# Kernel optimization log

Measured on AMD Instinct MI355X. Metric: run time of the kernel, lower is better.

The kernel has to match this reference:

```python
import jax, jax.numpy as jnp
import numpy as np

B, T, D = 2, 2048, 2048
H, KV = 16, 4
HD = D // H            # 128
N_REP = H // KV        # 4
KV_DIM = D * KV // H   # 512
ALIBI_W = 0.1


def _rotate_half(x):
    x1, x2 = jnp.split(x, 2, axis=-1)
    return jnp.concatenate([-x2, x1], axis=-1)


def _apply_rope(xq, xk, freqs_cis):
    # xq: [B,H,T,hd], xk: [B,KV,T,hd]; freqs_cis: [T, hd] (cos half | sin half)
    seq_len, head_dim = xq.shape[2], xq.shape[3]
    freqs = freqs_cis[:seq_len, :]
    half = head_dim // 2
    cos = jnp.repeat(freqs[:, :half], 2, axis=-1)[None, None]  # [1,1,T,hd]
    sin = jnp.repeat(freqs[:, half:], 2, axis=-1)[None, None]
    xq_out = xq * cos + _rotate_half(xq) * sin
    xk_out = xk * cos + _rotate_half(xk) * sin
    return xq_out, xk_out


def setup_inputs() -> dict:
    key = jax.random.key(0)
    ks = jax.random.split(key, 8)
    x = jax.random.normal(ks[0], (B, T, D), jnp.float32)
    # additive causal mask (0 on/below diag, -1e9 above)
    causal = jnp.tril(jnp.ones((T, T), jnp.bool_))
    mask = jnp.where(causal, 0.0, -1e9).astype(jnp.float32)[None, None]
    # RoPE table: first half cos, second half sin of t*theta
    inv_freq = 1.0 / (10000.0 ** (np.arange(0, HD, 2, dtype=np.float32) / HD))  # [hd/2]
    angles = jnp.arange(T, dtype=jnp.float32)[:, None] * jnp.asarray(inv_freq)[None, :]
    freqs_cis = jnp.concatenate([jnp.cos(angles), jnp.sin(angles)], axis=-1)  # [T, hd]
    # ALiBi bias: per-head slope * relative distance
    slopes = 2.0 ** (-8.0 * (jnp.arange(1, H + 1, dtype=jnp.float32) / H))  # [H]
    rel = (jnp.arange(T, dtype=jnp.float32)[None, :] - jnp.arange(T, dtype=jnp.float32)[:, None])
    alibi_bias = (-jnp.abs(rel)[None, None] * slopes[None, :, None, None]).astype(jnp.float32)
    std = 0.02
    Wq = std * jax.random.normal(ks[1], (D, D), jnp.float32)
    Wk = std * jax.random.normal(ks[2], (D, KV_DIM), jnp.float32)
    Wv = std * jax.random.normal(ks[3], (D, KV_DIM), jnp.float32)
    Wo = std * jax.random.normal(ks[4], (D, D), jnp.float32)
    return {"x": x, "mask": mask, "freqs_cis": freqs_cis, "alibi_bias": alibi_bias,
            "Wq": Wq, "Wk": Wk, "Wv": Wv, "Wo": Wo}


def reference(x, mask, freqs_cis, alibi_bias, Wq, Wk, Wv, Wo):
    b, t, d = x.shape
    q = (x @ Wq).reshape(b, t, H, HD).transpose(0, 2, 1, 3)      # [B,H,T,hd]
    k = (x @ Wk).reshape(b, t, KV, HD).transpose(0, 2, 1, 3)     # [B,KV,T,hd]
    v = (x @ Wv).reshape(b, t, KV, HD).transpose(0, 2, 1, 3)     # [B,KV,T,hd]
    q, k = _apply_rope(q, k, freqs_cis)
    # grouped-query scores: group query heads by kv head, avoid repeating K/V
    qg = q.reshape(b, KV, N_REP, t, HD)
    scores = jnp.einsum('bgrtd,bgsd->bgrts', qg, k) / jnp.sqrt(jnp.float32(HD))
    alibi = alibi_bias[:, :, :t, :t].reshape(1, KV, N_REP, t, t)
    scores = scores * (1.0 - ALIBI_W) + alibi * ALIBI_W
    scores = scores + mask[:, :, None, :t, :t]                   # broadcast [1,1,1,T,T]
    attn = jax.nn.softmax(scores.astype(jnp.float32), axis=-1).astype(x.dtype)
    out = jnp.einsum('bgrts,bgsd->bgrtd', attn, v)               # [B,KV,n_rep,T,hd]
    out = out.reshape(b, H, t, HD).transpose(0, 2, 1, 3).reshape(b, t, d)
    return out @ Wo
```

## Files before the change

kernel.cpp:

```cpp
#include <hip/hip_runtime.h>

#define T_SEQ 2048
#define D_MODEL 2048
#define NH 16
#define NKV 4
#define HEAD_DIM 128

typedef unsigned short u16;
typedef __attribute__((ext_vector_type(8))) short bf16x8;
typedef __attribute__((ext_vector_type(4))) float f32x4;

__device__ __forceinline__ float bf2f(u16 u) { return __uint_as_float(((unsigned)u) << 16); }
__device__ __forceinline__ u16 f2bf(float f) {
  unsigned x = __float_as_uint(f);
  return (u16)((x + 0x7FFFu + ((x >> 16) & 1u)) >> 16);
}
__device__ __forceinline__ float fexp2(float x) { return __builtin_amdgcn_exp2f(x); }

#define ASYNC_COPY16(g, l)                                                        \
  __builtin_amdgcn_global_load_lds((const __attribute__((address_space(1))) unsigned int*)(g), \
                                   (__attribute__((address_space(3))) unsigned int*)(l), 16, 0, 0)

#define BARRIER() do { asm volatile("" ::: "memory"); __builtin_amdgcn_s_barrier(); asm volatile("" ::: "memory"); } while (0)

template<int N> __device__ __forceinline__ void vmwait() {
  if constexpr (N == 0) asm volatile("s_waitcnt vmcnt(0)" ::: "memory");
  else if constexpr (N == 3) asm volatile("s_waitcnt vmcnt(3)" ::: "memory");
  else if constexpr (N == 4) asm volatile("s_waitcnt vmcnt(4)" ::: "memory");
  else if constexpr (N == 5) asm volatile("s_waitcnt vmcnt(5)" ::: "memory");
}

__global__ void cast_kernel(const float* __restrict__ x, u16* __restrict__ y, int n4) {
  int i = blockIdx.x * 256 + threadIdx.x;
  if (i >= n4) return;
  const float4 v = reinterpret_cast<const float4*>(x)[i];
  unsigned p0 = (unsigned)f2bf(v.x) | ((unsigned)f2bf(v.y) << 16);
  unsigned p1 = (unsigned)f2bf(v.z) | ((unsigned)f2bf(v.w) << 16);
  reinterpret_cast<uint2*>(y)[i] = make_uint2(p0, p1);
}

__global__ void transpose4_kernel(const float* __restrict__ Wq, const float* __restrict__ Wk,
                                  const float* __restrict__ Wv, const float* __restrict__ Wo,
                                  u16* __restrict__ qkvT, u16* __restrict__ WoT) {
  __shared__ float t[32][33];
  const int m = blockIdx.z;
  const float* W; u16* WT; int N;
  if (m == 0)      { W = Wq; WT = qkvT;                         N = 2048; }
  else if (m == 1) { W = Wk; WT = qkvT + (size_t)2048 * 2048;   N = 512;  }
  else if (m == 2) { W = Wv; WT = qkvT + (size_t)2560 * 2048;   N = 512;  }
  else             { W = Wo; WT = WoT;                          N = 2048; }
  const int n0 = blockIdx.x * 32, k0 = blockIdx.y * 32;
  if (n0 >= N) return;
  const int tx = threadIdx.x, ty = threadIdx.y;
#pragma unroll
  for (int i = 0; i < 32; i += 8)
    t[ty + i][tx] = W[(size_t)(k0 + ty + i) * N + n0 + tx];
  __syncthreads();
#pragma unroll
  for (int i = 0; i < 32; i += 8)
    WT[(size_t)(n0 + ty + i) * 2048 + k0 + tx] = f2bf(t[tx][ty + i]);
}

__global__ void vt_kernel(const u16* __restrict__ vb, u16* __restrict__ vt, int vstride) {
  __shared__ u16 t[32][33];
  const int bg = blockIdx.z;
  const int b = bg >> 2, g = bg & 3;
  const int t0 = blockIdx.x * 32, n0 = blockIdx.y * 32;
  const int tx = threadIdx.x, ty = threadIdx.y;
#pragma unroll
  for (int i = 0; i < 32; i += 8)
    t[ty + i][tx] = vb[((size_t)(b * T_SEQ + t0 + ty + i)) * vstride + g * HEAD_DIM + n0 + tx];
  __syncthreads();
#pragma unroll
  for (int i = 0; i < 32; i += 8)
    vt[((size_t)(bg * HEAD_DIM + n0 + ty + i)) * T_SEQ + t0 + tx] = t[tx][ty + i];
}

template<int BM, int BN, int WM, int WN, int EA, int EB, int OUT_BF16>
__global__ __launch_bounds__(512, 1) void gemm_dp(const u16* __restrict__ A, const u16* __restrict__ BT,
                                                  void* __restrict__ Cv, int M, int N, int K, int nbx) {
  constexpr int PA = BM / 64, PB = BN / 64;
  constexpr int E = EA + EB;
  constexpr int FM = BM / WM / 16, FN = BN / WN / 16;
  static_assert(FM % 2 == 0 && FN % 2 == 0, "quadrant split");
  __shared__ u16 SA[2][BM * 64];
  __shared__ u16 SB[2][BN * 64];
  const int tid = threadIdx.x;
  const int wave = tid >> 6, lane = tid & 63;
  const int lr = lane & 15, lg = lane >> 4;
  const int wm = wave / WN, wn = wave % WN;
  const int nwg = gridDim.x;
  const int bid = blockIdx.x;
  const int swz = (bid & 7) * (nwg >> 3) + (bid >> 3);
  const int bx = swz % nbx, by = swz / nbx;
  const size_t arow0 = (size_t)by * BM;
  const size_t brow0 = (size_t)bx * BN;
  const int NT = K >> 6;

  const int srow = tid >> 3;
  const int scol = ((tid & 7) ^ (srow & 7)) << 3;

  f32x4 acc[FM][FN] = {};
  bf16x8 af[FM / 2][2], bf0[FN / 2][2], bf1[FN / 2][2];

  const u16* Abase = A + arow0 * K;
  const u16* Bbase = BT + brow0 * K;

  auto stageA = [&](int p, int ktile, int buf) {
    if (ktile >= NT) return;
    const u16* src = Abase + (size_t)(p * 64 + srow) * K + (ktile << 6) + scol;
    ASYNC_COPY16(src, &SA[buf][(p * 64 + wave * 8) * 64]);
  };
  auto stageB = [&](int p, int ktile, int buf) {
    if (ktile >= NT) return;
    const u16* src = Bbase + (size_t)(p * 64 + srow) * K + (ktile << 6) + scol;
    ASYNC_COPY16(src, &SB[buf][(p * 64 + wave * 8) * 64]);
  };
  auto ldA = [&](int c, int mh) {
#pragma unroll
    for (int mf = 0; mf < FM / 2; ++mf)
#pragma unroll
      for (int ks = 0; ks < 2; ++ks) {
        const int row = wm * (BM / WM) + (mh * (FM / 2) + mf) * 16 + lr;
        const int slot = ((ks << 2) | lg) ^ (lr & 7);
        af[mf][ks] = *reinterpret_cast<const bf16x8*>(&SA[c][row * 64 + (slot << 3)]);
      }
  };
  auto ldB = [&](int c, int nh, bf16x8 (*bfr)[2]) {
#pragma unroll
    for (int nf = 0; nf < FN / 2; ++nf)
#pragma unroll
      for (int ks = 0; ks < 2; ++ks) {
        const int row = wn * (BN / WN) + (nh * (FN / 2) + nf) * 16 + lr;
        const int slot = ((ks << 2) | lg) ^ (lr & 7);
        bfr[nf][ks] = *reinterpret_cast<const bf16x8*>(&SB[c][row * 64 + (slot << 3)]);
      }
  };
  auto mq = [&](int mh, int nh, bf16x8 (*bfr)[2]) {
    __builtin_amdgcn_s_setprio(1);
#pragma unroll
    for (int mf = 0; mf < FM / 2; ++mf)
#pragma unroll
      for (int nf = 0; nf < FN / 2; ++nf)
#pragma unroll
        for (int ks = 0; ks < 2; ++ks)
          acc[mh * (FM / 2) + mf][nh * (FN / 2) + nf] = __builtin_amdgcn_mfma_f32_16x16x32_bf16(
              af[mf][ks], bfr[nf][ks], acc[mh * (FM / 2) + mf][nh * (FN / 2) + nf], 0, 0, 0);
    __builtin_amdgcn_s_setprio(0);
  };

#pragma unroll
  for (int p = 0; p < PA; ++p) stageA(p, 0, 0);
#pragma unroll
  for (int p = 0; p < PB; ++p) stageB(p, 0, 0);
#pragma unroll
  for (int p = 0; p < EB; ++p) stageB(p, 1, 1);
#pragma unroll
  for (int p = 0; p < EA; ++p) stageA(p, 1, 1);
  vmwait<E>();
  BARRIER();

  for (int kt = 0; kt < NT; ++kt) {
    const int c = kt & 1;
    ldA(c, 0); ldB(c, 0, bf0);
#pragma unroll
    for (int p = EB; p < PB; ++p) stageB(p, kt + 1, c ^ 1);
    BARRIER();
    mq(0, 0, bf0);
    BARRIER();
    ldB(c, 1, bf1);
#pragma unroll
    for (int p = EA; p < PA; ++p) stageA(p, kt + 1, c ^ 1);
    BARRIER();
    mq(0, 1, bf1);
    BARRIER();
    ldA(c, 1);
#pragma unroll
    for (int p = 0; p < EB; ++p) stageB(p, kt + 2, c);
    BARRIER();
    mq(1, 1, bf1);
    BARRIER();
#pragma unroll
    for (int p = 0; p < EA; ++p) stageA(p, kt + 2, c);
    BARRIER();
    mq(1, 0, bf0);
    if (kt + 2 < NT) vmwait<E>(); else vmwait<0>();
    BARRIER();
  }

#pragma unroll
  for (int mf = 0; mf < FM; ++mf)
#pragma unroll
    for (int nf = 0; nf < FN; ++nf)
#pragma unroll
      for (int r = 0; r < 4; ++r) {
        size_t row = arow0 + wm * (BM / WM) + mf * 16 + lg * 4 + r;
        size_t col = brow0 + wn * (BN / WN) + nf * 16 + lr;
        if (OUT_BF16) ((u16*)Cv)[row * N + col] = f2bf(acc[mf][nf][r]);
        else          ((float*)Cv)[row * N + col] = acc[mf][nf][r];
      }
}

__global__ void rope2_kernel(u16* __restrict__ qkv, const float* __restrict__ freqs) {
  const int QT = 4096 * NH * 64;
  int idx = blockIdx.x * 256 + threadIdx.x;
  u16* p; int log2nh;
  if (idx < QT) { p = qkv; log2nh = 4; }
  else          { p = qkv + 2048; log2nh = 2; idx -= QT; }
  int d = idx & 63;
  int h = (idx >> 6) & ((1 << log2nh) - 1);
  int row = idx >> (6 + log2nh);
  int t = row & (T_SEQ - 1);
  size_t base = (size_t)row * 3072 + (size_t)h * 128;
  float x1 = bf2f(p[base + d]);
  float x2 = bf2f(p[base + 64 + d]);
  const float* fr = freqs + (size_t)t * 128;
  int dh = d >> 1;
  float c1 = fr[dh],      s1 = fr[64 + dh];
  float c2 = fr[32 + dh], s2 = fr[96 + dh];
  p[base + d]      = f2bf(x1 * c1 - x2 * s1);
  p[base + 64 + d] = f2bf(x2 * c2 + x1 * s2);
}

__global__ __launch_bounds__(512) void attn_kernel(const u16* __restrict__ q, const u16* __restrict__ k,
                                                   const u16* __restrict__ vt, u16* __restrict__ o,
                                                   int qstride, int kstride) {
  __shared__ u16 Kl[2][64][136];
  __shared__ u16 Vl[2][128][72];
  __shared__ u16 Pl[8][16][72];
  const int b = blockIdx.z, h = blockIdx.y, pairIdx = blockIdx.x;
  const int g = h >> 2;
  const int tid = threadIdx.x, wave = tid >> 6, lane = tid & 63;
  const int lr = lane & 15, lg = lane >> 4;

  const float LOG2E = 1.44269504089f;
  const float qk_scale = 0.9f / sqrtf(128.f) * LOG2E;
  const float slope2   = 0.1f * fexp2(-0.5f * (h + 1)) * LOG2E;
  const float THR = 16.0f;

  const int krow = tid >> 3, kc0 = (tid & 7) * 16;
  const int vrow = tid >> 2, vc0 = (tid & 3) * 16;
  const u16* kbp = k + ((size_t)(b * T_SEQ + krow)) * kstride + g * HEAD_DIM + kc0;
  const u16* vbp = vt + ((size_t)((b * NKV + g) * HEAD_DIM + vrow)) * T_SEQ + vc0;

  float cb[4];
#pragma unroll
  for (int nt = 0; nt < 4; ++nt) cb[nt] = slope2 * (float)(nt * 16 + lr);

  for (int half = 0; half < 2; ++half) {
    const int qt = half ? (15 - pairIdx) : pairIdx;
    const int qbase = qt * 128;

    const u16* qp = q + ((size_t)(b * T_SEQ + qbase + wave * 16 + lr)) * qstride + h * HEAD_DIM;
    bf16x8 qf[4];
#pragma unroll
    for (int ks = 0; ks < 4; ++ks) qf[ks] = *reinterpret_cast<const bf16x8*>(qp + ks * 32 + lg * 8);

    f32x4 oa[8] = {};
    float m_r[4], l_r[4];
#pragma unroll
    for (int r = 0; r < 4; ++r) { m_r[r] = -1e30f; l_r[r] = 0.f; }

    const int ktmax = 2 * qt + 1;
    const int irow_min_w = qbase + wave * 16;
    const int irow_max_w = irow_min_w + 15;
    int cur = 0;

    __syncthreads();
    {
      bf16x8 k0a = *reinterpret_cast<const bf16x8*>(kbp);
      bf16x8 k0b = *reinterpret_cast<const bf16x8*>(kbp + 8);
      bf16x8 v0a = *reinterpret_cast<const bf16x8*>(vbp);
      bf16x8 v0b = *reinterpret_cast<const bf16x8*>(vbp + 8);
      *reinterpret_cast<bf16x8*>(&Kl[0][krow][kc0]) = k0a;
      *reinterpret_cast<bf16x8*>(&Kl[0][krow][kc0 + 8]) = k0b;
      *reinterpret_cast<bf16x8*>(&Vl[0][vrow][vc0]) = v0a;
      *reinterpret_cast<bf16x8*>(&Vl[0][vrow][vc0 + 8]) = v0b;
    }

    for (int kt = 0; kt <= ktmax; ++kt) {
      const int kbase = kt * 64;
      __syncthreads();

      const bool pf = (kt < ktmax);
      bf16x8 pk0, pk1, pv0, pv1;
      if (pf) {
        const u16* ks2p = kbp + (size_t)(kbase + 64) * kstride;
        pk0 = *reinterpret_cast<const bf16x8*>(ks2p);
        pk1 = *reinterpret_cast<const bf16x8*>(ks2p + 8);
        const u16* vs2p = vbp + kbase + 64;
        pv0 = *reinterpret_cast<const bf16x8*>(vs2p);
        pv1 = *reinterpret_cast<const bf16x8*>(vs2p + 8);
      }

      const bool compute = (kbase <= irow_max_w);
      if (compute) {
        f32x4 sa[4] = {};
#pragma unroll
        for (int nt = 0; nt < 4; ++nt)
#pragma unroll
          for (int ks = 0; ks < 4; ++ks)
            sa[nt] = __builtin_amdgcn_mfma_f32_16x16x32_bf16(
                qf[ks], *reinterpret_cast<const bf16x8*>(&Kl[cur][nt * 16 + lr][ks * 32 + lg * 8]), sa[nt], 0, 0, 0);

        const int i_row0 = irow_min_w + lg * 4;
        const float tb = slope2 * (float)kbase;
        float sv[4][4];
        float pmx[4] = {-1e30f, -1e30f, -1e30f, -1e30f};
        if (kbase + 63 <= irow_min_w) {
#pragma unroll
          for (int nt = 0; nt < 4; ++nt) {
            const float bias = cb[nt] + tb;
#pragma unroll
            for (int r = 0; r < 4; ++r) {
              float xv = fmaf(sa[nt][r], qk_scale, bias);
              sv[nt][r] = xv;
              pmx[r] = fmaxf(pmx[r], xv);
            }
          }
        } else {
#pragma unroll
          for (int nt = 0; nt < 4; ++nt) {
            const int jcol = kbase + nt * 16 + lr;
            const float bias = cb[nt] + tb;
#pragma unroll
            for (int r = 0; r < 4; ++r) {
              float xv = (jcol <= i_row0 + r) ? fmaf(sa[nt][r], qk_scale, bias) : -1e30f;
              sv[nt][r] = xv;
              pmx[r] = fmaxf(pmx[r], xv);
            }
          }
        }

        bool okl = true;
#pragma unroll
        for (int r = 0; r < 4; ++r) okl = okl && (pmx[r] <= m_r[r] + THR);
        if (__all(okl)) {
          float rs[4] = {0.f, 0.f, 0.f, 0.f};
#pragma unroll
          for (int nt = 0; nt < 4; ++nt)
#pragma unroll
            for (int r = 0; r < 4; ++r) {
              float p = fexp2(sv[nt][r] - m_r[r]);
              sv[nt][r] = p;
              rs[r] += p;
            }
#pragma unroll
          for (int r = 0; r < 4; ++r) l_r[r] += rs[r];
        } else {
#pragma unroll
          for (int mm = 1; mm < 16; mm <<= 1)
#pragma unroll
            for (int r = 0; r < 4; ++r) pmx[r] = fmaxf(pmx[r], __shfl_xor(pmx[r], mm, 64));
          float corr[4], rs[4];
#pragma unroll
          for (int r = 0; r < 4; ++r) {
            float mn = fmaxf(m_r[r], pmx[r]);
            corr[r] = fexp2(m_r[r] - mn);
            m_r[r] = mn;
            rs[r] = 0.f;
          }
#pragma unroll
          for (int nt = 0; nt < 4; ++nt)
#pragma unroll
            for (int r = 0; r < 4; ++r) {
              float p = fexp2(sv[nt][r] - m_r[r]);
              sv[nt][r] = p;
              rs[r] += p;
            }
#pragma unroll
          for (int r = 0; r < 4; ++r) l_r[r] = l_r[r] * corr[r] + rs[r];
#pragma unroll
          for (int t8 = 0; t8 < 8; ++t8)
#pragma unroll
            for (int r = 0; r < 4; ++r) oa[t8][r] *= corr[r];
        }

#pragma unroll
        for (int nt = 0; nt < 4; ++nt)
#pragma unroll
          for (int r = 0; r < 4; ++r)
            Pl[wave][lg * 4 + r][nt * 16 + lr] = f2bf(sv[nt][r]);
      }

      if (pf) {
        *reinterpret_cast<bf16x8*>(&Kl[cur ^ 1][krow][kc0]) = pk0;
        *reinterpret_cast<bf16x8*>(&Kl[cur ^ 1][krow][kc0 + 8]) = pk1;
        *reinterpret_cast<bf16x8*>(&Vl[cur ^ 1][vrow][vc0]) = pv0;
        *reinterpret_cast<bf16x8*>(&Vl[cur ^ 1][vrow][vc0 + 8]) = pv1;
      }

      if (compute) {
#pragma unroll
        for (int ht = 0; ht < 8; ++ht)
#pragma unroll
          for (int ks2 = 0; ks2 < 2; ++ks2) {
            bf16x8 pa = *reinterpret_cast<const bf16x8*>(&Pl[wave][lr][ks2 * 32 + lg * 8]);
            bf16x8 vb8 = *reinterpret_cast<const bf16x8*>(&Vl[cur][ht * 16 + lr][ks2 * 32 + lg * 8]);
            oa[ht] = __builtin_amdgcn_mfma_f32_16x16x32_bf16(pa, vb8, oa[ht], 0, 0, 0);
          }
      }
      cur ^= 1;
    }

#pragma unroll
    for (int mm = 1; mm < 16; mm <<= 1)
#pragma unroll
      for (int r = 0; r < 4; ++r) l_r[r] += __shfl_xor(l_r[r], mm, 64);

    u16* op = o + ((size_t)(b * T_SEQ + qbase + wave * 16)) * D_MODEL + h * HEAD_DIM;
#pragma unroll
    for (int r = 0; r < 4; ++r) {
      float inv = 1.0f / l_r[r];
#pragma unroll
      for (int ht = 0; ht < 8; ++ht)
        op[(size_t)(lg * 4 + r) * D_MODEL + ht * 16 + lr] = f2bf(oa[ht][r] * inv);
    }
  }
}

extern "C" void kernel_launch(void* const* d_in, const int* in_sizes, int n_in,
                              void* d_out, int out_size, void* d_ws, size_t ws_size,
                              hipStream_t stream) {
  (void)in_sizes; (void)n_in; (void)out_size; (void)ws_size;
  const float* x     = (const float*)d_in[0];
  const float* freqs = (const float*)d_in[2];
  const float* Wq    = (const float*)d_in[4];
  const float* Wk    = (const float*)d_in[5];
  const float* Wv    = (const float*)d_in[6];
  const float* Wo    = (const float*)d_in[7];
  float* out = (float*)d_out;
  char* ws = (char*)d_ws;
  const size_t MB = 1024 * 1024;
  u16* xb   = (u16*)(ws);
  u16* qkvT = (u16*)(ws + 16 * MB);
  u16* WoT  = (u16*)(ws + 28 * MB);
  u16* qkv  = (u16*)(ws + 36 * MB);
  u16* vtb  = (u16*)(ws + 16 * MB);
  const int M = 2 * T_SEQ;
  const int NQKV = 3072;

  cast_kernel<<<(M * D_MODEL / 4 + 255) / 256, 256, 0, stream>>>(x, xb, M * D_MODEL / 4);
  dim3 tb(32, 8);
  transpose4_kernel<<<dim3(64, 64, 4), tb, 0, stream>>>(Wq, Wk, Wv, Wo, qkvT, WoT);

  gemm_dp<256, 192, 4, 2, 2, 2, 1><<<256, 512, 0, stream>>>(xb, qkvT, qkv, M, NQKV, 2048, NQKV / 192);

  rope2_kernel<<<(M * NH * 64 + M * NKV * 64) / 256, 256, 0, stream>>>(qkv, freqs);

  vt_kernel<<<dim3(T_SEQ / 32, HEAD_DIM / 32, 2 * NKV), tb, 0, stream>>>(qkv + 2560, vtb, NQKV);

  attn_kernel<<<dim3(8, NH, 2), 512, 0, stream>>>(qkv, qkv + 2048, vtb, xb, NQKV, NQKV);

  gemm_dp<128, 256, 2, 4, 1, 2, 0><<<256, 512, 0, stream>>>(xb, WoT, out, M, 2048, 2048, 2048 / 256);
}
```

Before: 212.0 us.

## Process both paired query tiles in one K/V sweep to share loads

The attention kernel previously handled the two paired query tiles (pairIdx and 15-pairIdx) one after another, streaming K/V through LDS twice. Now both tiles' accumulators live in registers at once, and a single K/V loop up to the larger tile's causal limit serves both. The aim is to roughly halve K/V global loads, LDS fills and barriers for the shorter tile. The cost is doubled accumulator and Q register state (two sets of oa, m, l, qf), which raises register pressure and may reduce occupancy or cause spills.

```diff
diff --git a/kernel.cpp b/kernel.cpp
--- a/kernel.cpp
+++ b/kernel.cpp
@@ -247,175 +247,288 @@
 #pragma unroll
   for (int nt = 0; nt < 4; ++nt) cb[nt] = slope2 * (float)(nt * 16 + lr);
 
-  for (int half = 0; half < 2; ++half) {
-    const int qt = half ? (15 - pairIdx) : pairIdx;
-    const int qbase = qt * 128;
-
-    const u16* qp = q + ((size_t)(b * T_SEQ + qbase + wave * 16 + lr)) * qstride + h * HEAD_DIM;
-    bf16x8 qf[4];
-#pragma unroll
-    for (int ks = 0; ks < 4; ++ks) qf[ks] = *reinterpret_cast<const bf16x8*>(qp + ks * 32 + lg * 8);
-
-    f32x4 oa[8] = {};
-    float m_r[4], l_r[4];
-#pragma unroll
-    for (int r = 0; r < 4; ++r) { m_r[r] = -1e30f; l_r[r] = 0.f; }
-
-    const int ktmax = 2 * qt + 1;
-    const int irow_min_w = qbase + wave * 16;
-    const int irow_max_w = irow_min_w + 15;
-    int cur = 0;
-
+  const int qtA = pairIdx, qtB = 15 - pairIdx;
+  const int qbaseA = qtA * 128, qbaseB = qtB * 128;
+
+  const u16* qpA = q + ((size_t)(b * T_SEQ + qbaseA + wave * 16 + lr)) * qstride + h * HEAD_DIM;
+  const u16* qpB = q + ((size_t)(b * T_SEQ + qbaseB + wave * 16 + lr)) * qstride + h * HEAD_DIM;
+  bf16x8 qfA[4], qfB[4];
+#pragma unroll
+  for (int ks = 0; ks < 4; ++ks) {
+    qfA[ks] = *reinterpret_cast<const bf16x8*>(qpA + ks * 32 + lg * 8);
+    qfB[ks] = *reinterpret_cast<const bf16x8*>(qpB + ks * 32 + lg * 8);
+  }
+
+  f32x4 oaA[8] = {}, oaB[8] = {};
+  float mA[4], lA[4], mB[4], lB[4];
+#pragma unroll
+  for (int r = 0; r < 4; ++r) { mA[r] = -1e30f; lA[r] = 0.f; mB[r] = -1e30f; lB[r] = 0.f; }
+
+  const int ktmaxB = 2 * qtB + 1;
+  const int irowminA = qbaseA + wave * 16, irowmaxA = irowminA + 15;
+  const int irowminB = qbaseB + wave * 16, irowmaxB = irowminB + 15;
+  int cur = 0;
+
+  {
+    bf16x8 k0a = *reinterpret_cast<const bf16x8*>(kbp);
+    bf16x8 k0b = *reinterpret_cast<const bf16x8*>(kbp + 8);
+    bf16x8 v0a = *reinterpret_cast<const bf16x8*>(vbp);
+    bf16x8 v0b = *reinterpret_cast<const bf16x8*>(vbp + 8);
+    *reinterpret_cast<bf16x8*>(&Kl[0][krow][kc0]) = k0a;
+    *reinterpret_cast<bf16x8*>(&Kl[0][krow][kc0 + 8]) = k0b;
+    *reinterpret_cast<bf16x8*>(&Vl[0][vrow][vc0]) = v0a;
+    *reinterpret_cast<bf16x8*>(&Vl[0][vrow][vc0 + 8]) = v0b;
+  }
+
+  for (int kt = 0; kt <= ktmaxB; ++kt) {
+    const int kbase = kt * 64;
     __syncthreads();
-    {
-      bf16x8 k0a = *reinterpret_cast<const bf16x8*>(kbp);
-      bf16x8 k0b = *reinterpret_cast<const bf16x8*>(kbp + 8);
-      bf16x8 v0a = *reinterpret_cast<const bf16x8*>(vbp);
-      bf16x8 v0b = *reinterpret_cast<const bf16x8*>(vbp + 8);
-      *reinterpret_cast<bf16x8*>(&Kl[0][krow][kc0]) = k0a;
-      *reinterpret_cast<bf16x8*>(&Kl[0][krow][kc0 + 8]) = k0b;
-      *reinterpret_cast<bf16x8*>(&Vl[0][vrow][vc0]) = v0a;
-      *reinterpret_cast<bf16x8*>(&Vl[0][vrow][vc0 + 8]) = v0b;
+
+    const bool pf = (kt < ktmaxB);
+    bf16x8 pk0, pk1, pv0, pv1;
+    if (pf) {
+      const u16* ks2p = kbp + (size_t)(kbase + 64) * kstride;
+      pk0 = *reinterpret_cast<const bf16x8*>(ks2p);
+      pk1 = *reinterpret_cast<const bf16x8*>(ks2p + 8);
+      const u16* vs2p = vbp + kbase + 64;
+      pv0 = *reinterpret_cast<const bf16x8*>(vs2p);
+      pv1 = *reinterpret_cast<const bf16x8*>(vs2p + 8);
     }
 
-    for (int kt = 0; kt <= ktmax; ++kt) {
-      const int kbase = kt * 64;
-      __syncthreads();
-
-      const bool pf = (kt < ktmax);
-      bf16x8 pk0, pk1, pv0, pv1;
-      if (pf) {
-        const u16* ks2p = kbp + (size_t)(kbase + 64) * kstride;
-        pk0 = *reinterpret_cast<const bf16x8*>(ks2p);
-        pk1 = *reinterpret_cast<const bf16x8*>(ks2p + 8);
-        const u16* vs2p = vbp + kbase + 64;
-        pv0 = *reinterpret_cast<const bf16x8*>(vs2p);
-        pv1 = *reinterpret_cast<const bf16x8*>(vs2p + 8);
-      }
-
-      const bool compute = (kbase <= irow_max_w);
-      if (compute) {
-        f32x4 sa[4] = {};
+    const float tb = slope2 * (float)kbase;
+
+    const bool cA = (kbase <= irowmaxA);
+    if (cA) {
+      f32x4 sa[4] = {};
+#pragma unroll
+      for (int nt = 0; nt < 4; ++nt)
+#pragma unroll
+        for (int ks = 0; ks < 4; ++ks)
+          sa[nt] = __builtin_amdgcn_mfma_f32_16x16x32_bf16(
+              qfA[ks], *reinterpret_cast<const bf16x8*>(&Kl[cur][nt * 16 + lr][ks * 32 + lg * 8]), sa[nt], 0, 0, 0);
+
+      const int i_row0 = irowminA + lg * 4;
+      float sv[4][4];
+      float pmx[4] = {-1e30f, -1e30f, -1e30f, -1e30f};
+      if (kbase + 63 <= irowminA) {
+#pragma unroll
+        for (int nt = 0; nt < 4; ++nt) {
+          const float bias = cb[nt] + tb;
+#pragma unroll
+          for (int r = 0; r < 4; ++r) {
+            float xv = fmaf(sa[nt][r], qk_scale, bias);
+            sv[nt][r] = xv;
+            pmx[r] = fmaxf(pmx[r], xv);
+          }
+        }
+      } else {
+#pragma unroll
+        for (int nt = 0; nt < 4; ++nt) {
+          const int jcol = kbase + nt * 16 + lr;
+          const float bias = cb[nt] + tb;
+#pragma unroll
+          for (int r = 0; r < 4; ++r) {
+            float xv = (jcol <= i_row0 + r) ? fmaf(sa[nt][r], qk_scale, bias) : -1e30f;
+            sv[nt][r] = xv;
+            pmx[r] = fmaxf(pmx[r], xv);
+          }
+        }
+      }
+
+      bool okl = true;
+#pragma unroll
+      for (int r = 0; r < 4; ++r) okl = okl && (pmx[r] <= mA[r] + THR);
+      if (__all(okl)) {
+        float rs[4] = {0.f, 0.f, 0.f, 0.f};
 #pragma unroll
         for (int nt = 0; nt < 4; ++nt)
 #pragma unroll
-          for (int ks = 0; ks < 4; ++ks)
-            sa[nt] = __builtin_amdgcn_mfma_f32_16x16x32_bf16(
-                qf[ks], *reinterpret_cast<const bf16x8*>(&Kl[cur][nt * 16 + lr][ks * 32 + lg * 8]), sa[nt], 0, 0, 0);
-
-        const int i_row0 = irow_min_w + lg * 4;
-        const float tb = slope2 * (float)kbase;
-        float sv[4][4];
-        float pmx[4] = {-1e30f, -1e30f, -1e30f, -1e30f};
-        if (kbase + 63 <= irow_min_w) {
-#pragma unroll
-          for (int nt = 0; nt < 4; ++nt) {
-            const float bias = cb[nt] + tb;
-#pragma unroll
-            for (int r = 0; r < 4; ++r) {
-              float xv = fmaf(sa[nt][r], qk_scale, bias);
-              sv[nt][r] = xv;
-              pmx[r] = fmaxf(pmx[r], xv);
-            }
-          }
-        } else {
-#pragma unroll
-          for (int nt = 0; nt < 4; ++nt) {
-            const int jcol = kbase + nt * 16 + lr;
-            const float bias = cb[nt] + tb;
-#pragma unroll
-            for (int r = 0; r < 4; ++r) {
-              float xv = (jcol <= i_row0 + r) ? fmaf(sa[nt][r], qk_scale, bias) : -1e30f;
-              sv[nt][r] = xv;
-              pmx[r] = fmaxf(pmx[r], xv);
-            }
-          }
-        }
-
-        bool okl = true;
-#pragma unroll
-        for (int r = 0; r < 4; ++r) okl = okl && (pmx[r] <= m_r[r] + THR);
-        if (__all(okl)) {
-          float rs[4] = {0.f, 0.f, 0.f, 0.f};
-#pragma unroll
-          for (int nt = 0; nt < 4; ++nt)
-#pragma unroll
-            for (int r = 0; r < 4; ++r) {
-              float p = fexp2(sv[nt][r] - m_r[r]);
-              sv[nt][r] = p;
-              rs[r] += p;
-            }
-#pragma unroll
-          for (int r = 0; r < 4; ++r) l_r[r] += rs[r];
-        } else {
-#pragma unroll
-          for (int mm = 1; mm < 16; mm <<= 1)
-#pragma unroll
-            for (int r = 0; r < 4; ++r) pmx[r] = fmaxf(pmx[r], __shfl_xor(pmx[r], mm, 64));
-          float corr[4], rs[4];
-#pragma unroll
-          for (int r = 0; r < 4; ++r) {
-            float mn = fmaxf(m_r[r], pmx[r]);
-            corr[r] = fexp2(m_r[r] - mn);
-            m_r[r] = mn;
-            rs[r] = 0.f;
-          }
-#pragma unroll
-          for (int nt = 0; nt < 4; ++nt)
-#pragma unroll
-            for (int r = 0; r < 4; ++r) {
-              float p = fexp2(sv[nt][r] - m_r[r]);
-              sv[nt][r] = p;
-              rs[r] += p;
-            }
-#pragma unroll
-          for (int r = 0; r < 4; ++r) l_r[r] = l_r[r] * corr[r] + rs[r];
-#pragma unroll
-          for (int t8 = 0; t8 < 8; ++t8)
-#pragma unroll
-            for (int r = 0; r < 4; ++r) oa[t8][r] *= corr[r];
-        }
-
+          for (int r = 0; r < 4; ++r) {
+            float p = fexp2(sv[nt][r] - mA[r]);
+            sv[nt][r] = p;
+            rs[r] += p;
+          }
+#pragma unroll
+        for (int r = 0; r < 4; ++r) lA[r] += rs[r];
+      } else {
+#pragma unroll
+        for (int mm = 1; mm < 16; mm <<= 1)
+#pragma unroll
+          for (int r = 0; r < 4; ++r) pmx[r] = fmaxf(pmx[r], __shfl_xor(pmx[r], mm, 64));
+        float corr[4], rs[4];
+#pragma unroll
+        for (int r = 0; r < 4; ++r) {
+          float mn = fmaxf(mA[r], pmx[r]);
+          corr[r] = fexp2(mA[r] - mn);
+          mA[r] = mn;
+          rs[r] = 0.f;
+        }
 #pragma unroll
         for (int nt = 0; nt < 4; ++nt)
 #pragma unroll
-          for (int r = 0; r < 4; ++r)
-            Pl[wave][lg * 4 + r][nt * 16 + lr] = f2bf(sv[nt][r]);
-      }
-
-      if (pf) {
-        *reinterpret_cast<bf16x8*>(&Kl[cur ^ 1][krow][kc0]) = pk0;
-        *reinterpret_cast<bf16x8*>(&Kl[cur ^ 1][krow][kc0 + 8]) = pk1;
-        *reinterpret_cast<bf16x8*>(&Vl[cur ^ 1][vrow][vc0]) = pv0;
-        *reinterpret_cast<bf16x8*>(&Vl[cur ^ 1][vrow][vc0 + 8]) = pv1;
-      }
-
-      if (compute) {
-#pragma unroll
-        for (int ht = 0; ht < 8; ++ht)
-#pragma unroll
-          for (int ks2 = 0; ks2 < 2; ++ks2) {
-            bf16x8 pa = *reinterpret_cast<const bf16x8*>(&Pl[wave][lr][ks2 * 32 + lg * 8]);
-            bf16x8 vb8 = *reinterpret_cast<const bf16x8*>(&Vl[cur][ht * 16 + lr][ks2 * 32 + lg * 8]);
-            oa[ht] = __builtin_amdgcn_mfma_f32_16x16x32_bf16(pa, vb8, oa[ht], 0, 0, 0);
-          }
-      }
-      cur ^= 1;
+          for (int r = 0; r < 4; ++r) {
+            float p = fexp2(sv[nt][r] - mA[r]);
+            sv[nt][r] = p;
+            rs[r] += p;
+          }
+#pragma unroll
+        for (int r = 0; r < 4; ++r) lA[r] = lA[r] * corr[r] + rs[r];
+#pragma unroll
+        for (int t8 = 0; t8 < 8; ++t8)
+#pragma unroll
+          for (int r = 0; r < 4; ++r) oaA[t8][r] *= corr[r];
+      }
+
+#pragma unroll
+      for (int nt = 0; nt < 4; ++nt)
+#pragma unroll
+        for (int r = 0; r < 4; ++r)
+          Pl[wave][lg * 4 + r][nt * 16 + lr] = f2bf(sv[nt][r]);
     }
 
-#pragma unroll
-    for (int mm = 1; mm < 16; mm <<= 1)
-#pragma unroll
-      for (int r = 0; r < 4; ++r) l_r[r] += __shfl_xor(l_r[r], mm, 64);
-
-    u16* op = o + ((size_t)(b * T_SEQ + qbase + wave * 16)) * D_MODEL + h * HEAD_DIM;
-#pragma unroll
-    for (int r = 0; r < 4; ++r) {
-      float inv = 1.0f / l_r[r];
+    if (pf) {
+      *reinterpret_cast<bf16x8*>(&Kl[cur ^ 1][krow][kc0]) = pk0;
+      *reinterpret_cast<bf16x8*>(&Kl[cur ^ 1][krow][kc0 + 8]) = pk1;
+      *reinterpret_cast<bf16x8*>(&Vl[cur ^ 1][vrow][vc0]) = pv0;
+      *reinterpret_cast<bf16x8*>(&Vl[cur ^ 1][vrow][vc0 + 8]) = pv1;
+    }
+
+    if (cA) {
 #pragma unroll
       for (int ht = 0; ht < 8; ++ht)
-        op[(size_t)(lg * 4 + r) * D_MODEL + ht * 16 + lr] = f2bf(oa[ht][r] * inv);
+#pragma unroll
+        for (int ks2 = 0; ks2 < 2; ++ks2) {
+          bf16x8 pa = *reinterpret_cast<const bf16x8*>(&Pl[wave][lr][ks2 * 32 + lg * 8]);
+          bf16x8 vb8 = *reinterpret_cast<const bf16x8*>(&Vl[cur][ht * 16 + lr][ks2 * 32 + lg * 8]);
+          oaA[ht] = __builtin_amdgcn_mfma_f32_16x16x32_bf16(pa, vb8, oaA[ht], 0, 0, 0);
+        }
     }
+
+    const bool cB = (kbase <= irowmaxB);
+    if (cB) {
+      f32x4 sa[4] = {};
+#pragma unroll
+      for (int nt = 0; nt < 4; ++nt)
+#pragma unroll
+        for (int ks = 0; ks < 4; ++ks)
+          sa[nt] = __builtin_amdgcn_mfma_f32_16x16x32_bf16(
+              qfB[ks], *reinterpret_cast<const bf16x8*>(&Kl[cur][nt * 16 + lr][ks * 32 + lg * 8]), sa[nt], 0, 0, 0);
+
+      const int i_row0 = irowminB + lg * 4;
+      float sv[4][4];
+      float pmx[4] = {-1e30f, -1e30f, -1e30f, -1e30f};
+      if (kbase + 63 <= irowminB) {
+#pragma unroll
+        for (int nt = 0; nt < 4; ++nt) {
+          const float bias = cb[nt] + tb;
+#pragma unroll
+          for (int r = 0; r < 4; ++r) {
+            float xv = fmaf(sa[nt][r], qk_scale, bias);
+            sv[nt][r] = xv;
+            pmx[r] = fmaxf(pmx[r], xv);
+          }
+        }
+      } else {
+#pragma unroll
+        for (int nt = 0; nt < 4; ++nt) {
+          const int jcol = kbase + nt * 16 + lr;
+          const float bias = cb[nt] + tb;
+#pragma unroll
+          for (int r = 0; r < 4; ++r) {
+            float xv = (jcol <= i_row0 + r) ? fmaf(sa[nt][r], qk_scale, bias) : -1e30f;
+            sv[nt][r] = xv;
+            pmx[r] = fmaxf(pmx[r], xv);
+          }
+        }
+      }
+
+      bool okl = true;
+#pragma unroll
+      for (int r = 0; r < 4; ++r) okl = okl && (pmx[r] <= mB[r] + THR);
+      if (__all(okl)) {
+        float rs[4] = {0.f, 0.f, 0.f, 0.f};
+#pragma unroll
+        for (int nt = 0; nt < 4; ++nt)
+#pragma unroll
+          for (int r = 0; r < 4; ++r) {
+            float p = fexp2(sv[nt][r] - mB[r]);
+            sv[nt][r] = p;
+            rs[r] += p;
+          }
+#pragma unroll
+        for (int r = 0; r < 4; ++r) lB[r] += rs[r];
+      } else {
+#pragma unroll
+        for (int mm = 1; mm < 16; mm <<= 1)
+#pragma unroll
+          for (int r = 0; r < 4; ++r) pmx[r] = fmaxf(pmx[r], __shfl_xor(pmx[r], mm, 64));
+        float corr[4], rs[4];
+#pragma unroll
+        for (int r = 0; r < 4; ++r) {
+          float mn = fmaxf(mB[r], pmx[r]);
+          corr[r] = fexp2(mB[r] - mn);
+          mB[r] = mn;
+          rs[r] = 0.f;
+        }
+#pragma unroll
+        for (int nt = 0; nt < 4; ++nt)
+#pragma unroll
+          for (int r = 0; r < 4; ++r) {
+            float p = fexp2(sv[nt][r] - mB[r]);
+            sv[nt][r] = p;
+            rs[r] += p;
+          }
+#pragma unroll
+        for (int r = 0; r < 4; ++r) lB[r] = lB[r] * corr[r] + rs[r];
+#pragma unroll
+        for (int t8 = 0; t8 < 8; ++t8)
+#pragma unroll
+          for (int r = 0; r < 4; ++r) oaB[t8][r] *= corr[r];
+      }
+
+#pragma unroll
+      for (int nt = 0; nt < 4; ++nt)
+#pragma unroll
+        for (int r = 0; r < 4; ++r)
+          Pl[wave][lg * 4 + r][nt * 16 + lr] = f2bf(sv[nt][r]);
+
+#pragma unroll
+      for (int ht = 0; ht < 8; ++ht)
+#pragma unroll
+        for (int ks2 = 0; ks2 < 2; ++ks2) {
+          bf16x8 pa = *reinterpret_cast<const bf16x8*>(&Pl[wave][lr][ks2 * 32 + lg * 8]);
+          bf16x8 vb8 = *reinterpret_cast<const bf16x8*>(&Vl[cur][ht * 16 + lr][ks2 * 32 + lg * 8]);
+          oaB[ht] = __builtin_amdgcn_mfma_f32_16x16x32_bf16(pa, vb8, oaB[ht], 0, 0, 0);
+        }
+    }
+
+    cur ^= 1;
+  }
+
+#pragma unroll
+  for (int mm = 1; mm < 16; mm <<= 1)
+#pragma unroll
+    for (int r = 0; r < 4; ++r) lA[r] += __shfl_xor(lA[r], mm, 64);
+  u16* opA = o + ((size_t)(b * T_SEQ + qbaseA + wave * 16)) * D_MODEL + h * HEAD_DIM;
+#pragma unroll
+  for (int r = 0; r < 4; ++r) {
+    float inv = 1.0f / lA[r];
+#pragma unroll
+    for (int ht = 0; ht < 8; ++ht)
+      opA[(size_t)(lg * 4 + r) * D_MODEL + ht * 16 + lr] = f2bf(oaA[ht][r] * inv);
+  }
+
+#pragma unroll
+  for (int mm = 1; mm < 16; mm <<= 1)
+#pragma unroll
+    for (int r = 0; r < 4; ++r) lB[r] += __shfl_xor(lB[r], mm, 64);
+  u16* opB = o + ((size_t)(b * T_SEQ + qbaseB + wave * 16)) * D_MODEL + h * HEAD_DIM;
+#pragma unroll
+  for (int r = 0; r < 4; ++r) {
+    float inv = 1.0f / lB[r];
+#pragma unroll
+    for (int ht = 0; ht < 8; ++ht)
+      opB[(size_t)(lg * 4 + r) * D_MODEL + ht * 16 + lr] = f2bf(oaB[ht][r] * inv);
   }
 }
 
```

New measurement: 214.5 us. Within noise of the previous version (+1.2%).
